# Kernel optimization log

Hardware: AMD Instinct MI355X
Metric: run time of the kernel (lower is better)

The kernel has to match this reference:

```python
import jax, jax.numpy as jnp
import numpy as np

N_ITER = 4
NUM_BLOCKS = 8
EPS = 1.1920929e-07  # torch.finfo(float32).eps, default eps of F.rms_norm


def rmsnorm(x):
    ms = jnp.mean(jnp.square(x), axis=-1, keepdims=True)
    return x * jax.lax.rsqrt(ms + EPS)


def lslinear(x, W, A, B):
    # y = blockdiag(W) @ x + A @ B @ x
    *lead, fin = x.shape
    bi = fin // NUM_BLOCKS
    xb = x.reshape(*lead, NUM_BLOCKS, bi)
    Wb = W.reshape(NUM_BLOCKS, -1, bi)  # [nb, block_out, block_in]
    y = jnp.einsum('...ni,noi->...no', xb, Wb).reshape(*lead, -1)
    return y + (x @ B.T) @ A.T


def setup_inputs() -> dict:
    key = jax.random.key(0)
    ks = jax.random.split(key, 16)
    s = 0.02
    return {
        'x': jax.random.normal(ks[0], (8, 2048, 1024), jnp.float32),
        'fg_W': jax.random.normal(ks[1], (1024, 256), jnp.float32) * s,
        'fg_A': jax.random.normal(ks[2], (1024, 32), jnp.float32) * s,
        'fg_B': jax.random.normal(ks[3], (32, 2048), jnp.float32) * s,
        'gu_W': jax.random.normal(ks[4], (1024, 256), jnp.float32) * s,
        'gu_A': jax.random.normal(ks[5], (1024, 32), jnp.float32) * s,
        'gu_B': jax.random.normal(ks[6], (32, 2048), jnp.float32) * s,
        'ffg_W': jax.random.normal(ks[7], (2816, 128), jnp.float32) * s,
        'ffg_A': jax.random.normal(ks[8], (2816, 32), jnp.float32) * s,
        'ffg_B': jax.random.normal(ks[9], (32, 1024), jnp.float32) * s,
        'fff_W': jax.random.normal(ks[10], (2816, 128), jnp.float32) * s,
        'fff_A': jax.random.normal(ks[11], (2816, 32), jnp.float32) * s,
        'fff_B': jax.random.normal(ks[12], (32, 1024), jnp.float32) * s,
        'ffp_W': jax.random.normal(ks[13], (1024, 352), jnp.float32) * s,
        'ffp_A': jax.random.normal(ks[14], (1024, 32), jnp.float32) * s,
        'ffp_B': jax.random.normal(ks[15], (32, 2816), jnp.float32) * s,
    }


def reference(x, fg_W, fg_A, fg_B, gu_W, gu_A, gu_B,
              ffg_W, ffg_A, ffg_B, fff_W, fff_A, fff_B,
              ffp_W, ffp_A, ffp_B):
    h = x
    for _ in range(N_ITER):
        z = rmsnorm(h)
        # causal shift: token t sees token t-1 (zeros at t=0)
        shifted = jnp.concatenate([jnp.zeros_like(z[:, :1]), z[:, :-1]], axis=1)
        combined = jnp.concatenate([z, shifted], axis=-1)  # [B, S, 2d]
        gate = jax.nn.sigmoid(lslinear(combined, fg_W, fg_A, fg_B))
        update = lslinear(combined, gu_W, gu_A, gu_B)
        h = h + gate * update  # dropout p=0 -> identity
    z = rmsnorm(h)
    ff = jax.nn.silu(lslinear(z, ffg_W, ffg_A, ffg_B)) * lslinear(z, fff_W, fff_A, fff_B)
    return h + lslinear(ff, ffp_W, ffp_A, ffp_B)
```

## Files before the change

### kernel.cpp

```cpp
#include <hip/hip_runtime.h>
#include <hip/hip_bf16.h>
#include <hip/hip_fp16.h>

#define D     1024
#define D2    2048
#define S_LEN 2048
#define RANK  32
#define DFF   2816
#define EPS_F 1.1920929e-07f
#define T_IT  16
#define T_FN  8
#define ZPAD  1032
#define FPAD  2824

typedef unsigned short u16;
typedef unsigned int   u32;

__device__ __forceinline__ void unpack2(u32 u, float& lo, float& hi) {
    union { float f; u32 i; } a, b;
    a.i = u << 16;
    b.i = u & 0xFFFF0000u;
    lo = a.f; hi = b.f;
}

struct f8 { float v[8]; };
struct __align__(16) h8 { __half h[8]; };
struct __align__(8)  h4 { __half h[4]; };

template<bool F32>
__device__ __forceinline__ f8 load8(const void* base, size_t off) {
    f8 r;
    if (F32) {
        const float4* p = (const float4*)((const float*)base + off);
        float4 a = p[0], b = p[1];
        r.v[0]=a.x; r.v[1]=a.y; r.v[2]=a.z; r.v[3]=a.w;
        r.v[4]=b.x; r.v[5]=b.y; r.v[6]=b.z; r.v[7]=b.w;
    } else {
        uint4 u = *(const uint4*)((const u16*)base + off);
        unpack2(u.x, r.v[0], r.v[1]); unpack2(u.y, r.v[2], r.v[3]);
        unpack2(u.z, r.v[4], r.v[5]); unpack2(u.w, r.v[6], r.v[7]);
    }
    return r;
}

__device__ __forceinline__ f8 load8h(const __half* p) {
    h8 t = *(const h8*)p;
    f8 r;
    #pragma unroll
    for (int k = 0; k < 8; ++k) r.v[k] = __half2float(t.h[k]);
    return r;
}

template<bool F32>
__device__ __forceinline__ void load4(const void* base, size_t off,
                                      float& a0, float& a1, float& a2, float& a3) {
    if (F32) {
        float4 v = *(const float4*)((const float*)base + off);
        a0 = v.x; a1 = v.y; a2 = v.z; a3 = v.w;
    } else {
        uint2 v = *(const uint2*)((const u16*)base + off);
        unpack2(v.x, a0, a1); unpack2(v.y, a2, a3);
    }
}

template<bool F32>
__device__ __forceinline__ void load2(const void* base, size_t off, float& a0, float& a1) {
    if (F32) {
        float2 v = *(const float2*)((const float*)base + off);
        a0 = v.x; a1 = v.y;
    } else {
        u32 v = *(const u32*)((const u16*)base + off);
        unpack2(v, a0, a1);
    }
}

template<bool F32>
__device__ __forceinline__ float load1(const void* base, size_t off) {
    if (F32) return ((const float*)base)[off];
    u16 u = ((const u16*)base)[off];
    union { float f; u32 i; } a; a.i = ((u32)u) << 16;
    return a.f;
}

template<bool F32>
__device__ __forceinline__ void store1(void* base, size_t off, float v) {
    if (F32) ((float*)base)[off] = v;
    else     ((__hip_bfloat16*)base)[off] = __float2bfloat16(v);
}

__device__ __forceinline__ float dot8g(const f8& w, const float* __restrict__ x) {
    return w.v[0]*x[0] + w.v[1]*x[1] + w.v[2]*x[2] + w.v[3]*x[3]
         + w.v[4]*x[4] + w.v[5]*x[5] + w.v[6]*x[6] + w.v[7]*x[7];
}

__device__ __forceinline__ float dot8f(const f8& w, const f8& x) {
    return w.v[0]*x.v[0] + w.v[1]*x.v[1] + w.v[2]*x.v[2] + w.v[3]*x.v[3]
         + w.v[4]*x.v[4] + w.v[5]*x.v[5] + w.v[6]*x.v[6] + w.v[7]*x.v[7];
}

__device__ __forceinline__ float wave_reduce(float v) {
    #pragma unroll
    for (int off = 1; off < 64; off <<= 1)
        v += __shfl_xor(v, off, 64);
    return v;
}

__global__ void probe_kernel(const u32* __restrict__ x, int* __restrict__ flag) {
    __shared__ int cnt;
    int tid = threadIdx.x;
    if (tid == 0) cnt = 0;
    __syncthreads();
    u32 u = x[tid];
    float lo, hi; unpack2(u, lo, hi);
    int c = 0;
    if (!(fabsf(lo) < 1e4f)) c++;
    if (!(fabsf(hi) < 1e4f)) c++;
    if (c) atomicAdd(&cnt, c);
    __syncthreads();
    if (tid == 0) *flag = (cnt > 16) ? 1 : 0;
}

template<bool F32>
__global__ __launch_bounds__(512, 2) void iter_kernel(
    const int* __restrict__ flag,
    const void* __restrict__ hin, void* __restrict__ hout,
    const void* __restrict__ Wfg, const void* __restrict__ Afg, const void* __restrict__ Bfg,
    const void* __restrict__ Wgu, const void* __restrict__ Agu, const void* __restrict__ Bgu)
{
    if ((*flag != 0) != F32) return;

    __shared__ float Zl[T_IT + 1][ZPAD];
    __shared__ float tl[T_IT][2 * RANK];
    __shared__ float scl[T_IT + 1];

    const int tid = threadIdx.x;
    const int t0  = blockIdx.x * T_IT;
    const bool first = (t0 & (S_LEN - 1)) == 0;

    {
        const int c = tid * 2;
        for (int r = 0; r < T_IT + 1; ++r) {
            float a0 = 0.f, a1 = 0.f;
            if (r > 0 || !first)
                load2<F32>(hin, (size_t)(t0 - 1 + r) * D + c, a0, a1);
            Zl[r][c] = a0; Zl[r][c+1] = a1;
        }
    }
    __syncthreads();

    {
        const int wv = tid >> 6, ln = tid & 63;
        for (int r = wv; r < T_IT + 1; r += 8) {
            float ss = 0.f;
            #pragma unroll
            for (int k = 0; k < 4; ++k) {
                const float4 x = *(const float4*)&Zl[r][ln * 4 + k * 256];
                ss += x.x*x.x + x.y*x.y + x.z*x.z + x.w*x.w;
            }
            ss = wave_reduce(ss);
            if (ln == 0) scl[r] = rsqrtf(ss * (1.0f / 1024.0f) + EPS_F);
        }
    }
    __syncthreads();

    {
        const int c = tid * 2;
        for (int r = 0; r < T_IT + 1; ++r) {
            const float s = scl[r];
            float2* p = (float2*)&Zl[r][c];
            float2 x = *p;
            x.x *= s; x.y *= s;
            *p = x;
        }
    }
    __syncthreads();

    {
        const int g   = tid >> 3;
        const int sub = tid & 7;
        const void* Bm = (g < RANK) ? Bfg : Bgu;
        const int   gr = (g < RANK) ? g : g - RANK;
        const int   radd   = (sub < 4) ? 1 : 0;
        const int   coloff = (sub & 3) * 256;
        const size_t rbase = (size_t)gr * D2 + sub * 256;

        float acc[T_IT];
        #pragma unroll
        for (int t = 0; t < T_IT; ++t) acc[t] = 0.f;

        int cc = sub & 31;
        f8 w = load8<F32>(Bm, rbase + cc * 8);
        #pragma unroll 1
        for (int ii = 0; ii < 32; ++ii) {
            const f8 cw = w;
            const int ci = cc;
            if (ii < 31) {
                cc = (ii + 1 + sub) & 31;
                w = load8<F32>(Bm, rbase + cc * 8);
            }
            #pragma unroll
            for (int t = 0; t < T_IT; ++t)
                acc[t] += dot8g(cw, &Zl[t + radd][coloff + ci * 8]);
        }
        #pragma unroll
        for (int t = 0; t < T_IT; ++t) {
            float v = acc[t];
            v += __shfl_xor(v, 1, 64);
            v += __shfl_xor(v, 2, 64);
            v += __shfl_xor(v, 4, 64);
            if (sub == 0) tl[t][g] = v;
        }
    }
    __syncthreads();

    #pragma unroll 1
    for (int m = 0; m < 2; ++m) {
        const int o    = tid + m * 512;
        const int b    = o >> 7;
        const int radd = (b < 4) ? 1 : 0;
        const int col  = (b & 3) * 256;
        const size_t w0 = (size_t)o * 256;

        float af[T_IT], ag[T_IT];
        #pragma unroll
        for (int t = 0; t < T_IT; ++t) { af[t]=0.f; ag[t]=0.f; }

        f8 wf = load8<F32>(Wfg, w0);
        f8 wg = load8<F32>(Wgu, w0);
        #pragma unroll 1
        for (int i = 0; i < 32; ++i) {
            const f8 cf = wf, cg = wg;
            if (i < 31) {
                const int off = (i + 1) * 8;
                wf = load8<F32>(Wfg, w0 + off);
                wg = load8<F32>(Wgu, w0 + off);
            }
            const int xc = col + i * 8;
            #pragma unroll
            for (int t = 0; t < T_IT; ++t) {
                const float* x = &Zl[t + radd][xc];
                af[t] += dot8g(cf, x);
                ag[t] += dot8g(cg, x);
            }
        }

        #pragma unroll
        for (int rc = 0; rc < 4; ++rc) {
            const f8 a_f = load8<F32>(Afg, (size_t)o * RANK + rc * 8);
            const f8 a_g = load8<F32>(Agu, (size_t)o * RANK + rc * 8);
            #pragma unroll
            for (int t = 0; t < T_IT; ++t) {
                af[t] += dot8g(a_f, &tl[t][rc * 8]);
                ag[t] += dot8g(a_g, &tl[t][RANK + rc * 8]);
            }
        }

        #pragma unroll
        for (int t = 0; t < T_IT; ++t) {
            const float h = load1<F32>(hin, (size_t)(t0 + t) * D + o);
            const float gate = 1.f / (1.f + __expf(-af[t]));
            store1<F32>(hout, (size_t)(t0 + t) * D + o, h + gate * ag[t]);
        }
    }
}

template<bool F32>
__global__ __launch_bounds__(512, 2) void final_kernel(
    const int* __restrict__ flag,
    const void* __restrict__ hin, void* __restrict__ outp,
    const void* __restrict__ Wg, const void* __restrict__ Ag, const void* __restrict__ Bg,
    const void* __restrict__ Wf, const void* __restrict__ Af, const void* __restrict__ Bf,
    const void* __restrict__ Wp, const void* __restrict__ Ap, const void* __restrict__ Bp)
{
    if ((*flag != 0) != F32) return;

    __shared__ __align__(16) char smem[16512 + 45184];
    __half (*Zh)[ZPAD]  = (__half (*)[ZPAD])  smem;
    __half (*ffs)[FPAD] = (__half (*)[FPAD]) (smem + 16512);
    float* part2 = (float*)(smem + 16512);
    float* part4 = (float*)smem;

    __shared__ float tg[T_FN][RANK];
    __shared__ float tf[T_FN][RANK];
    __shared__ float tp[T_FN][RANK];
    __shared__ float red[8];

    const int tid = threadIdx.x;
    const int t0  = blockIdx.x * T_FN;
    const int wv  = tid >> 6;
    const int ln  = tid & 63;

    {
        float v[16];
        float ss = 0.f;
        #pragma unroll
        for (int k = 0; k < 4; ++k) {
            float a0, a1, a2, a3;
            load4<F32>(hin, (size_t)(t0 + wv) * D + ln * 4 + k * 256, a0, a1, a2, a3);
            v[k*4+0]=a0; v[k*4+1]=a1; v[k*4+2]=a2; v[k*4+3]=a3;
            ss += a0*a0 + a1*a1 + a2*a2 + a3*a3;
        }
        ss = wave_reduce(ss);
        const float sc = rsqrtf(ss * (1.0f / 1024.0f) + EPS_F);
        #pragma unroll
        for (int k = 0; k < 4; ++k) {
            h4 p;
            p.h[0] = __float2half(v[k*4+0]*sc);
            p.h[1] = __float2half(v[k*4+1]*sc);
            p.h[2] = __float2half(v[k*4+2]*sc);
            p.h[3] = __float2half(v[k*4+3]*sc);
            *(h4*)&Zh[wv][ln * 4 + k * 256] = p;
        }
    }
    __syncthreads();

    {
        const void* Bm = (ln < RANK) ? Bg : Bf;
        const int   gr = (ln < RANK) ? ln : ln - RANK;
        float acc[T_FN];
        #pragma unroll
        for (int t = 0; t < T_FN; ++t) acc[t] = 0.f;
        for (int cc = 0; cc < 16; ++cc) {
            const int c = wv * 128 + cc * 8;
            const f8 w = load8<F32>(Bm, (size_t)gr * D + c);
            #pragma unroll
            for (int t = 0; t < T_FN; ++t) {
                const f8 x = load8h(&Zh[t][c]);
                acc[t] += dot8f(w, x);
            }
        }
        #pragma unroll
        for (int t = 0; t < T_FN; ++t)
            part2[(wv * 8 + t) * 64 + ln] = acc[t];
    }
    __syncthreads();
    {
        const int t = tid >> 6, g = tid & 63;
        float s = 0.f;
        #pragma unroll
        for (int w = 0; w < 8; ++w) s += part2[(w * 8 + t) * 64 + g];
        if (g < RANK) tg[t][g] = s; else tf[t][g - RANK] = s;
    }
    __syncthreads();

    #pragma unroll 1
    for (int m = 0; m < 6; ++m) {
        const int j = tid + m * 512;
        if (j < DFF) {
            const int b  = j / 352;
            const int cb = b * 128;
            const size_t wr = (size_t)j * 128;
            float ag_[T_FN], af_[T_FN];
            #pragma unroll
            for (int t = 0; t < T_FN; ++t) { ag_[t] = 0.f; af_[t] = 0.f; }
            f8 wg8 = load8<F32>(Wg, wr), wf8 = load8<F32>(Wf, wr);
            #pragma unroll 1
            for (int i = 0; i < 16; ++i) {
                const f8 cg = wg8, cf = wf8;
                if (i < 15) {
                    wg8 = load8<F32>(Wg, wr + (i + 1) * 8);
                    wf8 = load8<F32>(Wf, wr + (i + 1) * 8);
                }
                #pragma unroll
                for (int t = 0; t < T_FN; ++t) {
                    const f8 x = load8h(&Zh[t][cb + i * 8]);
                    ag_[t] += dot8f(cg, x);
                    af_[t] += dot8f(cf, x);
                }
            }
            #pragma unroll
            for (int rc = 0; rc < 4; ++rc) {
                const f8 a_g = load8<F32>(Ag, (size_t)j * RANK + rc * 8);
                const f8 a_f = load8<F32>(Af, (size_t)j * RANK + rc * 8);
                #pragma unroll
                for (int t = 0; t < T_FN; ++t) {
                    ag_[t] += dot8g(a_g, &tg[t][rc * 8]);
                    af_[t] += dot8g(a_f, &tf[t][rc * 8]);
                }
            }
            #pragma unroll
            for (int t = 0; t < T_FN; ++t) {
                const float a = ag_[t];
                ffs[t][j] = __float2half((a / (1.f + __expf(-a))) * af_[t]);
            }
        }
    }
    __syncthreads();

    {
        const int seg = tid >> 5, r = tid & 31;
        float acc[T_FN];
        #pragma unroll
        for (int t = 0; t < T_FN; ++t) acc[t] = 0.f;
        for (int cc = 0; cc < 22; ++cc) {
            const int c = seg * 8 + cc * 128;
            const f8 w = load8<F32>(Bp, (size_t)r * DFF + c);
            #pragma unroll
            for (int t = 0; t < T_FN; ++t) {
                const f8 x = load8h(&ffs[t][c]);
                acc[t] += dot8f(w, x);
            }
        }
        #pragma unroll
        for (int t = 0; t < T_FN; ++t)
            part4[(seg * 8 + t) * 32 + r] = acc[t];
    }
    __syncthreads();
    if (tid < 256) {
        const int t = tid >> 5, r = tid & 31;
        float s = 0.f;
        #pragma unroll
        for (int sg = 0; sg < 16; ++sg) s += part4[(sg * 8 + t) * 32 + r];
        tp[t][r] = s;
    }
    __syncthreads();

    #pragma unroll 1
    for (int m = 0; m < 2; ++m) {
        const int o = tid + m * 512;
        const int b = o >> 7;
        const size_t wr = (size_t)o * 352;
        float acc[T_FN];
        #pragma unroll
        for (int t = 0; t < T_FN; ++t) acc[t] = 0.f;
        f8 w = load8<F32>(Wp, wr);
        #pragma unroll 1
        for (int i = 0; i < 44; ++i) {
            const f8 cw = w;
            if (i < 43) w = load8<F32>(Wp, wr + (i + 1) * 8);
            #pragma unroll
            for (int t = 0; t < T_FN; ++t) {
                const f8 x = load8h(&ffs[t][b * 352 + i * 8]);
                acc[t] += dot8f(cw, x);
            }
        }
        #pragma unroll
        for (int rc = 0; rc < 4; ++rc) {
            const f8 a8 = load8<F32>(Ap, (size_t)o * RANK + rc * 8);
            #pragma unroll
            for (int t = 0; t < T_FN; ++t)
                acc[t] += dot8g(a8, &tp[t][rc * 8]);
        }
        #pragma unroll
        for (int t = 0; t < T_FN; ++t) {
            const float h = load1<F32>(hin, (size_t)(t0 + t) * D + o);
            store1<F32>(outp, (size_t)(t0 + t) * D + o, h + acc[t]);
        }
    }
}

extern "C" void kernel_launch(void* const* d_in, const int* in_sizes, int n_in,
                              void* d_out, int out_size, void* d_ws, size_t ws_size,
                              hipStream_t stream) {
    const void* x     = d_in[0];
    const void* fg_W  = d_in[1];
    const void* fg_A  = d_in[2];
    const void* fg_B  = d_in[3];
    const void* gu_W  = d_in[4];
    const void* gu_A  = d_in[5];
    const void* gu_B  = d_in[6];
    const void* ffg_W = d_in[7];
    const void* ffg_A = d_in[8];
    const void* ffg_B = d_in[9];
    const void* fff_W = d_in[10];
    const void* fff_A = d_in[11];
    const void* fff_B = d_in[12];
    const void* ffp_W = d_in[13];
    const void* ffp_A = d_in[14];
    const void* ffp_B = d_in[15];

    int*  flag = (int*)d_ws;
    void* h1   = (void*)((char*)d_ws + 1024);
    void* hout = d_out;

    const int n_tok = 8 * S_LEN;

    probe_kernel<<<1, 256, 0, stream>>>((const u32*)x, flag);

    #define ITER(SRC, DST) \
        iter_kernel<false><<<n_tok / T_IT, 512, 0, stream>>>(flag, SRC, DST, fg_W, fg_A, fg_B, gu_W, gu_A, gu_B); \
        iter_kernel<true ><<<n_tok / T_IT, 512, 0, stream>>>(flag, SRC, DST, fg_W, fg_A, fg_B, gu_W, gu_A, gu_B);

    ITER(x,    h1)
    ITER(h1,   hout)
    ITER(hout, h1)
    ITER(h1,   hout)
    #undef ITER

    final_kernel<false><<<n_tok / T_FN, 512, 0, stream>>>(flag, hout, hout,
                                                          ffg_W, ffg_A, ffg_B,
                                                          fff_W, fff_A, fff_B,
                                                          ffp_W, ffp_A, ffp_B);
    final_kernel<true ><<<n_tok / T_FN, 512, 0, stream>>>(flag, hout, hout,
                                                          ffg_W, ffg_A, ffg_B,
                                                          fff_W, fff_A, fff_B,
                                                          ffp_W, ffp_A, ffp_B);
}
```

Baseline: 4.947 ms.

## Use fp16 shared activations and packed fdot2 dot products in all matvecs

Stores the normalized activations of the iteration kernel in shared memory as fp16 instead of fp32. Every inner dot product in both kernels now runs through the packed fp16 fdot2 instruction, converting weight vectors to half on the fly. This halves LDS footprint and traffic for Zl and doubles math throughput per instruction, at the cost of extra convert instructions and reduced precision in the recurrent h update. Before normalization the raw h values are now rounded to fp16, which risks overflow or precision loss.

```diff
diff --git a/kernel.cpp b/kernel.cpp
--- a/kernel.cpp
+++ b/kernel.cpp
@@ -15,6 +15,7 @@
 
 typedef unsigned short u16;
 typedef unsigned int   u32;
+typedef __fp16 hh2 __attribute__((ext_vector_type(2)));
 
 __device__ __forceinline__ void unpack2(u32 u, float& lo, float& hi) {
     union { float f; u32 i; } a, b;
@@ -24,7 +25,7 @@
 }
 
 struct f8 { float v[8]; };
-struct __align__(16) h8 { __half h[8]; };
+struct __align__(16) hv8 { hh2 p[4]; };
 struct __align__(8)  h4 { __half h[4]; };
 
 template<bool F32>
@@ -43,12 +44,34 @@
     return r;
 }
 
-__device__ __forceinline__ f8 load8h(const __half* p) {
-    h8 t = *(const h8*)p;
-    f8 r;
+__device__ __forceinline__ hv8 cvt8h(const f8& w) {
+    hv8 r;
     #pragma unroll
-    for (int k = 0; k < 8; ++k) r.v[k] = __half2float(t.h[k]);
+    for (int k = 0; k < 4; ++k) {
+        hh2 t;
+        t[0] = (__fp16)w.v[2*k];
+        t[1] = (__fp16)w.v[2*k+1];
+        r.p[k] = t;
+    }
     return r;
+}
+
+__device__ __forceinline__ hv8 loadh8(const __half* p) {
+    return *(const hv8*)p;
+}
+
+__device__ __forceinline__ float dot8h(const hv8& w, const hv8& x, float acc) {
+#if __has_builtin(__builtin_amdgcn_fdot2)
+    acc = __builtin_amdgcn_fdot2(w.p[0], x.p[0], acc, false);
+    acc = __builtin_amdgcn_fdot2(w.p[1], x.p[1], acc, false);
+    acc = __builtin_amdgcn_fdot2(w.p[2], x.p[2], acc, false);
+    acc = __builtin_amdgcn_fdot2(w.p[3], x.p[3], acc, false);
+#else
+    #pragma unroll
+    for (int k = 0; k < 4; ++k)
+        acc += (float)w.p[k][0]*(float)x.p[k][0] + (float)w.p[k][1]*(float)x.p[k][1];
+#endif
+    return acc;
 }
 
 template<bool F32>
@@ -93,11 +116,6 @@
          + w.v[4]*x[4] + w.v[5]*x[5] + w.v[6]*x[6] + w.v[7]*x[7];
 }
 
-__device__ __forceinline__ float dot8f(const f8& w, const f8& x) {
-    return w.v[0]*x.v[0] + w.v[1]*x.v[1] + w.v[2]*x.v[2] + w.v[3]*x.v[3]
-         + w.v[4]*x.v[4] + w.v[5]*x.v[5] + w.v[6]*x.v[6] + w.v[7]*x.v[7];
-}
-
 __device__ __forceinline__ float wave_reduce(float v) {
     #pragma unroll
     for (int off = 1; off < 64; off <<= 1)
@@ -129,7 +147,7 @@
 {
     if ((*flag != 0) != F32) return;
 
-    __shared__ float Zl[T_IT + 1][ZPAD];
+    __shared__ __half Zl[T_IT + 1][ZPAD];
     __shared__ float tl[T_IT][2 * RANK];
     __shared__ float scl[T_IT + 1];
 
@@ -143,7 +161,8 @@
             float a0 = 0.f, a1 = 0.f;
             if (r > 0 || !first)
                 load2<F32>(hin, (size_t)(t0 - 1 + r) * D + c, a0, a1);
-            Zl[r][c] = a0; Zl[r][c+1] = a1;
+            hh2 pk; pk[0] = (__fp16)a0; pk[1] = (__fp16)a1;
+            *(hh2*)&Zl[r][c] = pk;
         }
     }
     __syncthreads();
@@ -153,9 +172,9 @@
         for (int r = wv; r < T_IT + 1; r += 8) {
             float ss = 0.f;
             #pragma unroll
-            for (int k = 0; k < 4; ++k) {
-                const float4 x = *(const float4*)&Zl[r][ln * 4 + k * 256];
-                ss += x.x*x.x + x.y*x.y + x.z*x.z + x.w*x.w;
+            for (int k = 0; k < 2; ++k) {
+                const hv8 x = loadh8(&Zl[r][ln * 8 + k * 512]);
+                ss = dot8h(x, x, ss);
             }
             ss = wave_reduce(ss);
             if (ln == 0) scl[r] = rsqrtf(ss * (1.0f / 1024.0f) + EPS_F);
@@ -167,10 +186,9 @@
         const int c = tid * 2;
         for (int r = 0; r < T_IT + 1; ++r) {
             const float s = scl[r];
-            float2* p = (float2*)&Zl[r][c];
-            float2 x = *p;
-            x.x *= s; x.y *= s;
-            *p = x;
+            hh2 v = *(hh2*)&Zl[r][c];
+            hh2 o; o[0] = (__fp16)((float)v[0] * s); o[1] = (__fp16)((float)v[1] * s);
+            *(hh2*)&Zl[r][c] = o;
         }
     }
     __syncthreads();
@@ -192,7 +210,7 @@
         f8 w = load8<F32>(Bm, rbase + cc * 8);
         #pragma unroll 1
         for (int ii = 0; ii < 32; ++ii) {
-            const f8 cw = w;
+            const hv8 cw = cvt8h(w);
             const int ci = cc;
             if (ii < 31) {
                 cc = (ii + 1 + sub) & 31;
@@ -200,7 +218,7 @@
             }
             #pragma unroll
             for (int t = 0; t < T_IT; ++t)
-                acc[t] += dot8g(cw, &Zl[t + radd][coloff + ci * 8]);
+                acc[t] = dot8h(cw, loadh8(&Zl[t + radd][coloff + ci * 8]), acc[t]);
         }
         #pragma unroll
         for (int t = 0; t < T_IT; ++t) {
@@ -225,22 +243,22 @@
         #pragma unroll
         for (int t = 0; t < T_IT; ++t) { af[t]=0.f; ag[t]=0.f; }
 
-        f8 wf = load8<F32>(Wfg, w0);
-        f8 wg = load8<F32>(Wgu, w0);
+        f8 wfr = load8<F32>(Wfg, w0);
+        f8 wgr = load8<F32>(Wgu, w0);
         #pragma unroll 1
         for (int i = 0; i < 32; ++i) {
-            const f8 cf = wf, cg = wg;
+            const hv8 cf = cvt8h(wfr), cg = cvt8h(wgr);
             if (i < 31) {
                 const int off = (i + 1) * 8;
-                wf = load8<F32>(Wfg, w0 + off);
-                wg = load8<F32>(Wgu, w0 + off);
+                wfr = load8<F32>(Wfg, w0 + off);
+                wgr = load8<F32>(Wgu, w0 + off);
             }
             const int xc = col + i * 8;
             #pragma unroll
             for (int t = 0; t < T_IT; ++t) {
-                const float* x = &Zl[t + radd][xc];
-                af[t] += dot8g(cf, x);
-                ag[t] += dot8g(cg, x);
+                const hv8 x = loadh8(&Zl[t + radd][xc]);
+                af[t] = dot8h(cf, x, af[t]);
+                ag[t] = dot8h(cg, x, ag[t]);
             }
         }
 
@@ -280,10 +298,9 @@
     float* part2 = (float*)(smem + 16512);
     float* part4 = (float*)smem;
 
-    __shared__ float tg[T_FN][RANK];
-    __shared__ float tf[T_FN][RANK];
-    __shared__ float tp[T_FN][RANK];
-    __shared__ float red[8];
+    __shared__ float tg_[T_FN][RANK];
+    __shared__ float tf_[T_FN][RANK];
+    __shared__ float tp_[T_FN][RANK];
 
     const int tid = threadIdx.x;
     const int t0  = blockIdx.x * T_FN;
@@ -322,12 +339,10 @@
         for (int t = 0; t < T_FN; ++t) acc[t] = 0.f;
         for (int cc = 0; cc < 16; ++cc) {
             const int c = wv * 128 + cc * 8;
-            const f8 w = load8<F32>(Bm, (size_t)gr * D + c);
-            #pragma unroll
-            for (int t = 0; t < T_FN; ++t) {
-                const f8 x = load8h(&Zh[t][c]);
-                acc[t] += dot8f(w, x);
-            }
+            const hv8 w = cvt8h(load8<F32>(Bm, (size_t)gr * D + c));
+            #pragma unroll
+            for (int t = 0; t < T_FN; ++t)
+                acc[t] = dot8h(w, loadh8(&Zh[t][c]), acc[t]);
         }
         #pragma unroll
         for (int t = 0; t < T_FN; ++t)
@@ -339,7 +354,7 @@
         float s = 0.f;
         #pragma unroll
         for (int w = 0; w < 8; ++w) s += part2[(w * 8 + t) * 64 + g];
-        if (g < RANK) tg[t][g] = s; else tf[t][g - RANK] = s;
+        if (g < RANK) tg_[t][g] = s; else tf_[t][g - RANK] = s;
     }
     __syncthreads();
 
@@ -356,16 +371,16 @@
             f8 wg8 = load8<F32>(Wg, wr), wf8 = load8<F32>(Wf, wr);
             #pragma unroll 1
             for (int i = 0; i < 16; ++i) {
-                const f8 cg = wg8, cf = wf8;
+                const hv8 cg = cvt8h(wg8), cf = cvt8h(wf8);
                 if (i < 15) {
                     wg8 = load8<F32>(Wg, wr + (i + 1) * 8);
                     wf8 = load8<F32>(Wf, wr + (i + 1) * 8);
                 }
                 #pragma unroll
                 for (int t = 0; t < T_FN; ++t) {
-                    const f8 x = load8h(&Zh[t][cb + i * 8]);
-                    ag_[t] += dot8f(cg, x);
-                    af_[t] += dot8f(cf, x);
+                    const hv8 x = loadh8(&Zh[t][cb + i * 8]);
+                    ag_[t] = dot8h(cg, x, ag_[t]);
+                    af_[t] = dot8h(cf, x, af_[t]);
                 }
             }
             #pragma unroll
@@ -374,8 +389,8 @@
                 const f8 a_f = load8<F32>(Af, (size_t)j * RANK + rc * 8);
                 #pragma unroll
                 for (int t = 0; t < T_FN; ++t) {
-                    ag_[t] += dot8g(a_g, &tg[t][rc * 8]);
-                    af_[t] += dot8g(a_f, &tf[t][rc * 8]);
+                    ag_[t] += dot8g(a_g, &tg_[t][rc * 8]);
+                    af_[t] += dot8g(a_f, &tf_[t][rc * 8]);
                 }
             }
             #pragma unroll
@@ -394,12 +409,10 @@
         for (int t = 0; t < T_FN; ++t) acc[t] = 0.f;
         for (int cc = 0; cc < 22; ++cc) {
             const int c = seg * 8 + cc * 128;
-            const f8 w = load8<F32>(Bp, (size_t)r * DFF + c);
-            #pragma unroll
-            for (int t = 0; t < T_FN; ++t) {
-                const f8 x = load8h(&ffs[t][c]);
-                acc[t] += dot8f(w, x);
-            }
+            const hv8 w = cvt8h(load8<F32>(Bp, (size_t)r * DFF + c));
+            #pragma unroll
+            for (int t = 0; t < T_FN; ++t)
+                acc[t] = dot8h(w, loadh8(&ffs[t][c]), acc[t]);
         }
         #pragma unroll
         for (int t = 0; t < T_FN; ++t)
@@ -411,7 +424,7 @@
         float s = 0.f;
         #pragma unroll
         for (int sg = 0; sg < 16; ++sg) s += part4[(sg * 8 + t) * 32 + r];
-        tp[t][r] = s;
+        tp_[t][r] = s;
     }
     __syncthreads();
 
@@ -426,20 +439,18 @@
         f8 w = load8<F32>(Wp, wr);
         #pragma unroll 1
         for (int i = 0; i < 44; ++i) {
-            const f8 cw = w;
+            const hv8 cw = cvt8h(w);
             if (i < 43) w = load8<F32>(Wp, wr + (i + 1) * 8);
             #pragma unroll
-            for (int t = 0; t < T_FN; ++t) {
-                const f8 x = load8h(&ffs[t][b * 352 + i * 8]);
-                acc[t] += dot8f(cw, x);
-            }
+            for (int t = 0; t < T_FN; ++t)
+                acc[t] = dot8h(cw, loadh8(&ffs[t][b * 352 + i * 8]), acc[t]);
         }
         #pragma unroll
         for (int rc = 0; rc < 4; ++rc) {
             const f8 a8 = load8<F32>(Ap, (size_t)o * RANK + rc * 8);
             #pragma unroll
             for (int t = 0; t < T_FN; ++t)
-                acc[t] += dot8g(a8, &tp[t][rc * 8]);
+                acc[t] += dot8g(a8, &tp_[t][rc * 8]);
         }
         #pragma unroll
         for (int t = 0; t < T_FN; ++t) {
```

New measurement: 4.491 ms. 1.1x faster.
